# Optimization experiments

Measured on AMD Instinct MI355X. Metric: run time of the kernel, lower is better.

## Reference

```python
import jax, jax.numpy as jnp
import numpy as np

B_SZ, L, D, N = 4, 2048, 768, 16


def setup_inputs() -> dict:
    key = jax.random.key(0)
    ks = jax.random.split(key, 8)
    x = jax.random.normal(ks[0], (B_SZ, L, D), dtype=jnp.float32)
    # A_log initialized as log(arange(1..N)) repeated over d, as in the module
    A_log = jnp.log(jnp.broadcast_to(jnp.arange(1, N + 1, dtype=jnp.float32), (D, N)))
    # s_b_c: Linear(D, 2N)
    W_bc = jax.random.normal(ks[1], (2 * N, D), dtype=jnp.float32) / jnp.sqrt(D)
    b_bc = jnp.zeros((2 * N,), dtype=jnp.float32)
    # s_1: Linear(D, 1)
    W_1 = jax.random.normal(ks[2], (1, D), dtype=jnp.float32) / jnp.sqrt(D)
    b_1 = jnp.zeros((1,), dtype=jnp.float32)
    # s_delta: Linear(1, D)
    W_d = jax.random.normal(ks[3], (D, 1), dtype=jnp.float32)
    b_d = jnp.zeros((D,), dtype=jnp.float32)
    return {"x": x, "A_log": A_log, "W_bc": W_bc, "b_bc": b_bc,
            "W_1": W_1, "b_1": b_1, "W_d": W_d, "b_d": b_d}


def reference(x, A_log, W_bc, b_bc, W_1, b_1, W_d, b_d):
    b, l, d = x.shape
    n = A_log.shape[1]
    A = -jnp.exp(A_log)                                   # (d, n)
    BandC = x @ W_bc.T + b_bc                             # (b, l, 2n)
    Bm, Cm = BandC[..., :n], BandC[..., n:]               # (b, l, n) each
    # delta = softplus(s_delta(s_1(x)))  -> (b, l, d)
    s1 = x @ W_1.T + b_1                                  # (b, l, 1)
    delta = jax.nn.softplus(s1 @ W_d.T + b_d)             # (b, l, d)
    deltaA = jnp.exp(jnp.einsum('bld,dn->bldn', delta, A))        # (b, l, d, n)
    deltaB_u = jnp.einsum('bld,bln,bld->bldn', delta, Bm, x)      # (b, l, d, n)

    # sequential selective-scan over time with lax.scan
    dA_t = jnp.moveaxis(deltaA, 1, 0)      # (l, b, d, n)
    dBu_t = jnp.moveaxis(deltaB_u, 1, 0)   # (l, b, d, n)
    C_t = jnp.moveaxis(Cm, 1, 0)           # (l, b, n)

    def step(h, inp):
        dA_i, dBu_i, c_i = inp
        h = dA_i * h + dBu_i               # (b, d, n)
        y = jnp.einsum('bdn,bn->bd', h, c_i)
        return h, y

    h0 = jnp.zeros((b, d, n), dtype=x.dtype)
    _, ys = jax.lax.scan(step, h0, (dA_t, dBu_t, C_t))
    return jnp.moveaxis(ys, 0, 1)          # (b, l, d)
```

## Files before the change

kernel.cpp:

```cpp
#include <hip/hip_runtime.h>
#include <hip/hip_cooperative_groups.h>

namespace cg = cooperative_groups;

#define L_SEQ 2048
#define D_DIM 768
#define N_ST 16
#define NB 4
#define NJ 33
#define BCS 48
#define NROWS (NB * L_SEQ)
#define PROJ_ELEMS (NROWS * NJ)
#define DN (D_DIM * N_ST)

#define NCC 64
#define LCC 32
#define GS  768
#define SEGC 4
#define SCC 16

#define DSPLIT 8
#define DSEG (D_DIM / DSPLIT)
#define DK 32
#define NCHUNK (DSEG / DK)
#define RB 128
#define XST 132
#define WST 64

typedef float v2f __attribute__((ext_vector_type(2)));

__device__ __forceinline__ float fast_exp2(float x) {
#if __has_builtin(__builtin_amdgcn_exp2f)
  return __builtin_amdgcn_exp2f(x);
#else
  return __expf(x * 0.69314718055994531f);
#endif
}

__device__ __forceinline__ float softplus_f(float v) {
  float e = fast_exp2(v * 1.44269504088896f);
  float l = __log2f(1.0f + e) * 0.69314718055994531f;
  return (v > 15.0f) ? v : l;
}

__device__ __forceinline__ void pow_tree2(float e1, v2f pw2[8]) {
  float e2s = e1 * e1;
  float e4s = e2s * e2s;
  float e8s = e4s * e4s;
  v2f s2 = {e2s, e2s}, s4 = {e4s, e4s}, s8 = {e8s, e8s};
  pw2[0] = (v2f){e1, e2s};
  pw2[1] = pw2[0] * s2;
  pw2[2] = pw2[0] * s4;
  pw2[3] = pw2[1] * s4;
  pw2[4] = pw2[0] * s8;
  pw2[5] = pw2[1] * s8;
  pw2[6] = pw2[2] * s8;
  pw2[7] = pw2[3] * s8;
}

__global__ __launch_bounds__(256) void k_proj_gemm(
    const float* __restrict__ x, const float* __restrict__ W_bc,
    const float* __restrict__ W_1, float* __restrict__ PBC) {
  __shared__ float xs_t[DK * XST];
  __shared__ float ws_t[DK * WST];

  const int ds  = blockIdx.x % DSPLIT;
  const int rb0 = (blockIdx.x / DSPLIT) * RB;
  const int dbase = ds * DSEG;
  const int tid = threadIdx.x;
  const int rg = tid & 31;
  const int jg = tid >> 5;

  float acc[4][5];
#pragma unroll
  for (int i = 0; i < 4; ++i)
#pragma unroll
    for (int k = 0; k < 5; ++k) acc[i][k] = 0.0f;

  const int lrow = tid >> 1;
  const int lhalf = (tid & 1) * 16;
  const float* xg_row = x + (size_t)(rb0 + lrow) * D_DIM + dbase + lhalf;

  for (int ch = 0; ch < NCHUNK; ++ch) {
    const int dc = dbase + ch * DK;
    float4 xv[4];
#pragma unroll
    for (int q = 0; q < 4; ++q)
      xv[q] = *(const float4*)(xg_row + ch * DK + q * 4);
    float wv[8];
    int widx[8];
#pragma unroll
    for (int u = 0; u < 8; ++u) {
      int idx = tid + u * 256;
      int dk = idx >> 6, slot = idx & 63;
      int wjg = slot >> 3, wk = slot & 7;
      int j = wjg + 8 * wk;
      float v = 0.0f;
      if (wk < 5) {
        if (j < 32)       v = W_bc[(size_t)j * D_DIM + dc + dk];
        else if (j == 32) v = W_1[dc + dk];
      }
      wv[u] = v; widx[u] = dk * WST + slot;
    }
    __syncthreads();
#pragma unroll
    for (int q = 0; q < 4; ++q) {
      xs_t[(lhalf + q * 4 + 0) * XST + lrow] = xv[q].x;
      xs_t[(lhalf + q * 4 + 1) * XST + lrow] = xv[q].y;
      xs_t[(lhalf + q * 4 + 2) * XST + lrow] = xv[q].z;
      xs_t[(lhalf + q * 4 + 3) * XST + lrow] = xv[q].w;
    }
#pragma unroll
    for (int u = 0; u < 8; ++u) ws_t[widx[u]] = wv[u];
    __syncthreads();
#pragma unroll 8
    for (int dk = 0; dk < DK; ++dk) {
      float4 xr = *(const float4*)&xs_t[dk * XST + rg * 4];
      float4 wr = *(const float4*)&ws_t[dk * WST + jg * 8];
      float w4  = ws_t[dk * WST + jg * 8 + 4];
      float xa[4] = {xr.x, xr.y, xr.z, xr.w};
      float wa[5] = {wr.x, wr.y, wr.z, wr.w, w4};
#pragma unroll
      for (int i = 0; i < 4; ++i)
#pragma unroll
        for (int k = 0; k < 5; ++k)
          acc[i][k] = fmaf(xa[i], wa[k], acc[i][k]);
    }
  }

  float* pb = PBC + (size_t)ds * PROJ_ELEMS;
#pragma unroll
  for (int i = 0; i < 4; ++i) {
    int row = rb0 + rg * 4 + i;
#pragma unroll
    for (int k = 0; k < 5; ++k) {
      int j = jg + 8 * k;
      if (k < 4 || jg == 0) pb[(size_t)row * NJ + j] = acc[i][k];
    }
  }
}

__device__ __forceinline__ void phase_reduce(
    const float* __restrict__ PBC, const float* __restrict__ b_bc,
    const float* __restrict__ b_1, float* __restrict__ BC48) {
  const int t0 = blockIdx.x * 256 + threadIdx.x;
  for (int idx = t0; idx < PROJ_ELEMS; idx += GS * 256) {
    const int row = idx / NJ;
    const int j = idx - row * NJ;
    float s = 0.0f;
#pragma unroll
    for (int k = 0; k < DSPLIT; ++k) s += PBC[(size_t)k * PROJ_ELEMS + idx];
    s += (j < 32) ? b_bc[j] : b_1[0];
    BC48[(size_t)row * BCS + j] = s;
  }
}

__device__ __forceinline__ void phase_scan1(
    const float* __restrict__ x, const float* __restrict__ A_log,
    const float* __restrict__ W_d, const float* __restrict__ b_d,
    const float* __restrict__ BC48, float* __restrict__ DS,
    float* __restrict__ H) {
  const int cb = blockIdx.x % 3;
  const int c  = (blockIdx.x / 3) % NCC;
  const int b  = blockIdx.x / (3 * NCC);
  const int d  = cb * 256 + threadIdx.x;

  const float wd = W_d[d], bd = b_d[d];
  float Aln[N_ST];
  {
    const float4* al4 = (const float4*)(A_log + (size_t)d * N_ST);
#pragma unroll
    for (int q = 0; q < 4; ++q) {
      float4 v = al4[q];
      Aln[4*q+0] = -__expf(v.x) * 1.44269504088896f;
      Aln[4*q+1] = -__expf(v.y) * 1.44269504088896f;
      Aln[4*q+2] = -__expf(v.z) * 1.44269504088896f;
      Aln[4*q+3] = -__expf(v.w) * 1.44269504088896f;
    }
  }
  bool geom = true;
#pragma unroll
  for (int n = 1; n < N_ST; ++n) {
    float ref = (float)(n + 1) * Aln[0];
    geom = geom && (fabsf(Aln[n] - ref) <= 1e-4f * fabsf(ref) + 1e-12f);
  }
  const float a0 = Aln[0];

  v2f h2[8];
#pragma unroll
  for (int k = 0; k < 8; ++k) h2[k] = (v2f){0.0f, 0.0f};
  float dsum = 0.0f;

  const int l0 = c * LCC;
  const float* bc = BC48 + (size_t)(b * L_SEQ + l0) * BCS;
  const float* xp = x + (size_t)(b * L_SEQ + l0) * D_DIM + d;

  if (geom) {
#pragma unroll 8
    for (int l = 0; l < LCC; ++l) {
      const float* r = bc + l * BCS;
      float4 B0 = *(const float4*)(r + 0);
      float4 B1 = *(const float4*)(r + 4);
      float4 B2 = *(const float4*)(r + 8);
      float4 B3 = *(const float4*)(r + 12);
      float s1 = r[32];
      float delta = softplus_f(fmaf(s1, wd, bd));
      float xv = xp[(size_t)l * D_DIM];
      float f = delta * xv;
      dsum += delta;
      v2f pw2[8];
      pow_tree2(fast_exp2(a0 * delta), pw2);
      v2f f2 = {f, f};
      h2[0] = pw2[0] * h2[0] + f2 * (v2f){B0.x, B0.y};
      h2[1] = pw2[1] * h2[1] + f2 * (v2f){B0.z, B0.w};
      h2[2] = pw2[2] * h2[2] + f2 * (v2f){B1.x, B1.y};
      h2[3] = pw2[3] * h2[3] + f2 * (v2f){B1.z, B1.w};
      h2[4] = pw2[4] * h2[4] + f2 * (v2f){B2.x, B2.y};
      h2[5] = pw2[5] * h2[5] + f2 * (v2f){B2.z, B2.w};
      h2[6] = pw2[6] * h2[6] + f2 * (v2f){B3.x, B3.y};
      h2[7] = pw2[7] * h2[7] + f2 * (v2f){B3.z, B3.w};
    }
  } else {
#pragma unroll 4
    for (int l = 0; l < LCC; ++l) {
      const float* r = bc + l * BCS;
      float s1 = r[32];
      float delta = softplus_f(fmaf(s1, wd, bd));
      float f = delta * xp[(size_t)l * D_DIM];
      dsum += delta;
#pragma unroll
      for (int k = 0; k < 8; ++k) {
        h2[k].x = fmaf(fast_exp2(delta * Aln[2*k]),   h2[k].x, f * r[2*k]);
        h2[k].y = fmaf(fast_exp2(delta * Aln[2*k+1]), h2[k].y, f * r[2*k+1]);
      }
    }
  }

  DS[((size_t)b * NCC + c) * D_DIM + d] = dsum;
  size_t base = ((size_t)(b * NCC + c) * D_DIM + d) * N_ST;
  float4* H4 = (float4*)(H + base);
#pragma unroll
  for (int q = 0; q < 4; ++q)
    H4[q] = make_float4(h2[2*q].x, h2[2*q].y, h2[2*q+1].x, h2[2*q+1].y);
}

__device__ __forceinline__ void phase_combine(
    const float* __restrict__ A_log, const float* __restrict__ DS,
    float* __restrict__ H) {
  __shared__ float Pl[SEGC * 65];
  __shared__ float Hl[SEGC * 65];
  const int b    = blockIdx.x / 192;
  const int dn0  = (blockIdx.x % 192) * 64;
  const int lane = threadIdx.x & 63;
  const int j    = threadIdx.x >> 6;
  const int dn   = dn0 + lane;
  const int d    = dn >> 4;

  const float Aln1 = -__expf(A_log[dn]) * 1.44269504088896f;

  const float* dsp = DS + (size_t)b * NCC * D_DIM + d;
  float* Hp = H + (size_t)b * NCC * DN + dn;

  float p[SCC], ph[SCC];
#pragma unroll
  for (int k = 0; k < SCC; ++k) {
    const int c = j * SCC + k;
    p[k]  = fast_exp2(Aln1 * dsp[(size_t)c * D_DIM]);
    ph[k] = Hp[(size_t)c * DN];
  }

  float Pagg = 1.0f, Hagg = 0.0f;
#pragma unroll
  for (int k = 0; k < SCC; ++k) {
    Hagg = fmaf(p[k], Hagg, ph[k]);
    Pagg *= p[k];
  }

  Pl[j * 65 + lane] = Pagg;
  Hl[j * 65 + lane] = Hagg;
  __syncthreads();

  float h = 0.0f;
  for (int j2 = 0; j2 < j; ++j2)
    h = fmaf(Pl[j2 * 65 + lane], h, Hl[j2 * 65 + lane]);

#pragma unroll
  for (int k = 0; k < SCC; ++k) {
    Hp[(size_t)(j * SCC + k) * DN] = h;
    h = fmaf(p[k], h, ph[k]);
  }
}

__device__ __forceinline__ void phase_scan2(
    const float* __restrict__ x, const float* __restrict__ A_log,
    const float* __restrict__ W_d, const float* __restrict__ b_d,
    const float* __restrict__ BC48, const float* __restrict__ HIN,
    float* __restrict__ out) {
  const int cb = blockIdx.x % 3;
  const int c  = (blockIdx.x / 3) % NCC;
  const int b  = blockIdx.x / (3 * NCC);
  const int d  = cb * 256 + threadIdx.x;

  const float wd = W_d[d], bd = b_d[d];
  float Aln[N_ST];
  {
    const float4* al4 = (const float4*)(A_log + (size_t)d * N_ST);
#pragma unroll
    for (int q = 0; q < 4; ++q) {
      float4 v = al4[q];
      Aln[4*q+0] = -__expf(v.x) * 1.44269504088896f;
      Aln[4*q+1] = -__expf(v.y) * 1.44269504088896f;
      Aln[4*q+2] = -__expf(v.z) * 1.44269504088896f;
      Aln[4*q+3] = -__expf(v.w) * 1.44269504088896f;
    }
  }
  bool geom = true;
#pragma unroll
  for (int n = 1; n < N_ST; ++n) {
    float ref = (float)(n + 1) * Aln[0];
    geom = geom && (fabsf(Aln[n] - ref) <= 1e-4f * fabsf(ref) + 1e-12f);
  }
  const float a0 = Aln[0];

  v2f h2[8];
  {
    size_t base = ((size_t)(b * NCC + c) * D_DIM + d) * N_ST;
    const float4* HIN4 = (const float4*)(HIN + base);
#pragma unroll
    for (int q = 0; q < 4; ++q) {
      float4 v = HIN4[q];
      h2[2*q]   = (v2f){v.x, v.y};
      h2[2*q+1] = (v2f){v.z, v.w};
    }
  }

  const int l0 = c * LCC;
  const float* bc = BC48 + (size_t)(b * L_SEQ + l0) * BCS;
  const float* xp = x + (size_t)(b * L_SEQ + l0) * D_DIM + d;
  float* op = out + (size_t)(b * L_SEQ + l0) * D_DIM + d;

  if (geom) {
#pragma unroll 8
    for (int l = 0; l < LCC; ++l) {
      const float* r = bc + l * BCS;
      float4 B0 = *(const float4*)(r + 0);
      float4 B1 = *(const float4*)(r + 4);
      float4 B2 = *(const float4*)(r + 8);
      float4 B3 = *(const float4*)(r + 12);
      float4 C0 = *(const float4*)(r + 16);
      float4 C1 = *(const float4*)(r + 20);
      float4 C2 = *(const float4*)(r + 24);
      float4 C3 = *(const float4*)(r + 28);
      float s1 = r[32];
      float delta = softplus_f(fmaf(s1, wd, bd));
      float xv = xp[(size_t)l * D_DIM];
      float f = delta * xv;
      v2f pw2[8];
      pow_tree2(fast_exp2(a0 * delta), pw2);
      v2f f2 = {f, f};
      v2f y2 = {0.0f, 0.0f};
      h2[0] = pw2[0] * h2[0] + f2 * (v2f){B0.x, B0.y};  y2 += h2[0] * (v2f){C0.x, C0.y};
      h2[1] = pw2[1] * h2[1] + f2 * (v2f){B0.z, B0.w};  y2 += h2[1] * (v2f){C0.z, C0.w};
      h2[2] = pw2[2] * h2[2] + f2 * (v2f){B1.x, B1.y};  y2 += h2[2] * (v2f){C1.x, C1.y};
      h2[3] = pw2[3] * h2[3] + f2 * (v2f){B1.z, B1.w};  y2 += h2[3] * (v2f){C1.z, C1.w};
      h2[4] = pw2[4] * h2[4] + f2 * (v2f){B2.x, B2.y};  y2 += h2[4] * (v2f){C2.x, C2.y};
      h2[5] = pw2[5] * h2[5] + f2 * (v2f){B2.z, B2.w};  y2 += h2[5] * (v2f){C2.z, C2.w};
      h2[6] = pw2[6] * h2[6] + f2 * (v2f){B3.x, B3.y};  y2 += h2[6] * (v2f){C3.x, C3.y};
      h2[7] = pw2[7] * h2[7] + f2 * (v2f){B3.z, B3.w};  y2 += h2[7] * (v2f){C3.z, C3.w};
      op[(size_t)l * D_DIM] = y2.x + y2.y;
    }
  } else {
#pragma unroll 4
    for (int l = 0; l < LCC; ++l) {
      const float* r = bc + l * BCS;
      float s1 = r[32];
      float delta = softplus_f(fmaf(s1, wd, bd));
      float f = delta * xp[(size_t)l * D_DIM];
      float y = 0.0f;
#pragma unroll
      for (int k = 0; k < 8; ++k) {
        h2[k].x = fmaf(fast_exp2(delta * Aln[2*k]),   h2[k].x, f * r[2*k]);
        h2[k].y = fmaf(fast_exp2(delta * Aln[2*k+1]), h2[k].y, f * r[2*k+1]);
        y = fmaf(h2[k].x, r[16 + 2*k], y);
        y = fmaf(h2[k].y, r[16 + 2*k + 1], y);
      }
      op[(size_t)l * D_DIM] = y;
    }
  }
}

__global__ __launch_bounds__(256, 3) void k_mega(
    const float* __restrict__ x, const float* __restrict__ A_log,
    const float* __restrict__ W_d, const float* __restrict__ b_d,
    const float* __restrict__ PBC, const float* __restrict__ b_bc,
    const float* __restrict__ b_1, float* __restrict__ BC48,
    float* __restrict__ DS, float* __restrict__ H, float* __restrict__ out) {
  cg::grid_group grid = cg::this_grid();
  phase_reduce(PBC, b_bc, b_1, BC48);
  grid.sync();
  phase_scan1(x, A_log, W_d, b_d, BC48, DS, H);
  grid.sync();
  phase_combine(A_log, DS, H);
  grid.sync();
  phase_scan2(x, A_log, W_d, b_d, BC48, H, out);
}

__global__ __launch_bounds__(256) void k_reduce_f(
    const float* __restrict__ PBC, const float* __restrict__ b_bc,
    const float* __restrict__ b_1, float* __restrict__ BC48) {
  phase_reduce(PBC, b_bc, b_1, BC48);
}
__global__ __launch_bounds__(256, 3) void k_scan1_f(
    const float* __restrict__ x, const float* __restrict__ A_log,
    const float* __restrict__ W_d, const float* __restrict__ b_d,
    const float* __restrict__ BC48, float* __restrict__ DS,
    float* __restrict__ H) {
  phase_scan1(x, A_log, W_d, b_d, BC48, DS, H);
}
__global__ __launch_bounds__(256) void k_combine_f(
    const float* __restrict__ A_log, const float* __restrict__ DS,
    float* __restrict__ H) {
  phase_combine(A_log, DS, H);
}
__global__ __launch_bounds__(256, 3) void k_scan2_f(
    const float* __restrict__ x, const float* __restrict__ A_log,
    const float* __restrict__ W_d, const float* __restrict__ b_d,
    const float* __restrict__ BC48, const float* __restrict__ HIN,
    float* __restrict__ out) {
  phase_scan2(x, A_log, W_d, b_d, BC48, HIN, out);
}

extern "C" void kernel_launch(void* const* d_in, const int* in_sizes, int n_in,
                              void* d_out, int out_size, void* d_ws, size_t ws_size,
                              hipStream_t stream) {
  const float* x     = (const float*)d_in[0];
  const float* A_log = (const float*)d_in[1];
  const float* W_bc  = (const float*)d_in[2];
  const float* b_bc  = (const float*)d_in[3];
  const float* W_1   = (const float*)d_in[4];
  const float* b_1   = (const float*)d_in[5];
  const float* W_d   = (const float*)d_in[6];
  const float* b_d   = (const float*)d_in[7];
  float* out = (float*)d_out;
  float* ws  = (float*)d_ws;

  float* BC48 = ws;
  float* PBC  = BC48 + (size_t)NROWS * BCS;
  float* DSb  = PBC + (size_t)DSPLIT * PROJ_ELEMS;
  float* H    = DSb + (size_t)NB * NCC * D_DIM;

  k_proj_gemm<<<(NROWS / RB) * DSPLIT, 256, 0, stream>>>(x, W_bc, W_1, PBC);

  static int coop = -1;
  if (coop < 0) {
    int dev = 0;
    (void)hipGetDevice(&dev);
    int v = 0;
    (void)hipDeviceGetAttribute(&v, hipDeviceAttributeCooperativeLaunch, dev);
    coop = v ? 1 : 0;
  }

  if (coop == 1) {
    void* args[] = {(void*)&x, (void*)&A_log, (void*)&W_d, (void*)&b_d,
                    (void*)&PBC, (void*)&b_bc, (void*)&b_1,
                    (void*)&BC48, (void*)&DSb, (void*)&H, (void*)&out};
    hipError_t e = hipLaunchCooperativeKernel((const void*)k_mega, dim3(GS),
                                              dim3(256), args, 0, stream);
    if (e == hipSuccess) return;
    coop = 0;
  }

  k_reduce_f<<<GS, 256, 0, stream>>>(PBC, b_bc, b_1, BC48);
  k_scan1_f<<<GS, 256, 0, stream>>>(x, A_log, W_d, b_d, BC48, DSb, H);
  k_combine_f<<<GS, 256, 0, stream>>>(A_log, DSb, H);
  k_scan2_f<<<GS, 256, 0, stream>>>(x, A_log, W_d, b_d, BC48, H, out);
}
```

Baseline: 151.6 us.

## Reuse chunk-local outputs in scan2 and move projection reduce out of cooperative kernel

```diff
diff --git a/kernel.cpp b/kernel.cpp
--- a/kernel.cpp
+++ b/kernel.cpp
@@ -140,18 +140,63 @@
   }
 }
 
-__device__ __forceinline__ void phase_reduce(
+__global__ __launch_bounds__(256) void k_proj_reduce(
     const float* __restrict__ PBC, const float* __restrict__ b_bc,
     const float* __restrict__ b_1, float* __restrict__ BC48) {
-  const int t0 = blockIdx.x * 256 + threadIdx.x;
-  for (int idx = t0; idx < PROJ_ELEMS; idx += GS * 256) {
-    const int row = idx / NJ;
-    const int j = idx - row * NJ;
-    float s = 0.0f;
-#pragma unroll
-    for (int k = 0; k < DSPLIT; ++k) s += PBC[(size_t)k * PROJ_ELEMS + idx];
-    s += (j < 32) ? b_bc[j] : b_1[0];
-    BC48[(size_t)row * BCS + j] = s;
+  const int idx = blockIdx.x * 256 + threadIdx.x;
+  const int row = idx / NJ;
+  const int j = idx - row * NJ;
+  float s = 0.0f;
+#pragma unroll
+  for (int k = 0; k < DSPLIT; ++k) s += PBC[(size_t)k * PROJ_ELEMS + idx];
+  s += (j < 32) ? b_bc[j] : b_1[0];
+  BC48[(size_t)row * BCS + j] = s;
+}
+
+__device__ __forceinline__ void phase_combine(
+    const float* __restrict__ A_log, const float* __restrict__ DS,
+    float* __restrict__ H) {
+  __shared__ float Pl[SEGC * 65];
+  __shared__ float Hl[SEGC * 65];
+  const int b    = blockIdx.x / 192;
+  const int dn0  = (blockIdx.x % 192) * 64;
+  const int lane = threadIdx.x & 63;
+  const int j    = threadIdx.x >> 6;
+  const int dn   = dn0 + lane;
+  const int d    = dn >> 4;
+
+  const float Aln1 = -__expf(A_log[dn]) * 1.44269504088896f;
+
+  const float* dsp = DS + (size_t)b * NCC * D_DIM + d;
+  float* Hp = H + (size_t)b * NCC * DN + dn;
+
+  float p[SCC], ph[SCC];
+#pragma unroll
+  for (int k = 0; k < SCC; ++k) {
+    const int c = j * SCC + k;
+    p[k]  = fast_exp2(Aln1 * dsp[(size_t)c * D_DIM]);
+    ph[k] = Hp[(size_t)c * DN];
+  }
+
+  float Pagg = 1.0f, Hagg = 0.0f;
+#pragma unroll
+  for (int k = 0; k < SCC; ++k) {
+    Hagg = fmaf(p[k], Hagg, ph[k]);
+    Pagg *= p[k];
+  }
+
+  Pl[j * 65 + lane] = Pagg;
+  Hl[j * 65 + lane] = Hagg;
+  __syncthreads();
+
+  float h = 0.0f;
+  for (int j2 = 0; j2 < j; ++j2)
+    h = fmaf(Pl[j2 * 65 + lane], h, Hl[j2 * 65 + lane]);
+
+#pragma unroll
+  for (int k = 0; k < SCC; ++k) {
+    Hp[(size_t)(j * SCC + k) * DN] = h;
+    h = fmaf(p[k], h, ph[k]);
   }
 }
 
@@ -242,53 +287,6 @@
 #pragma unroll
   for (int q = 0; q < 4; ++q)
     H4[q] = make_float4(h2[2*q].x, h2[2*q].y, h2[2*q+1].x, h2[2*q+1].y);
-}
-
-__device__ __forceinline__ void phase_combine(
-    const float* __restrict__ A_log, const float* __restrict__ DS,
-    float* __restrict__ H) {
-  __shared__ float Pl[SEGC * 65];
-  __shared__ float Hl[SEGC * 65];
-  const int b    = blockIdx.x / 192;
-  const int dn0  = (blockIdx.x % 192) * 64;
-  const int lane = threadIdx.x & 63;
-  const int j    = threadIdx.x >> 6;
-  const int dn   = dn0 + lane;
-  const int d    = dn >> 4;
-
-  const float Aln1 = -__expf(A_log[dn]) * 1.44269504088896f;
-
-  const float* dsp = DS + (size_t)b * NCC * D_DIM + d;
-  float* Hp = H + (size_t)b * NCC * DN + dn;
-
-  float p[SCC], ph[SCC];
-#pragma unroll
-  for (int k = 0; k < SCC; ++k) {
-    const int c = j * SCC + k;
-    p[k]  = fast_exp2(Aln1 * dsp[(size_t)c * D_DIM]);
-    ph[k] = Hp[(size_t)c * DN];
-  }
-
-  float Pagg = 1.0f, Hagg = 0.0f;
-#pragma unroll
-  for (int k = 0; k < SCC; ++k) {
-    Hagg = fmaf(p[k], Hagg, ph[k]);
-    Pagg *= p[k];
-  }
-
-  Pl[j * 65 + lane] = Pagg;
-  Hl[j * 65 + lane] = Hagg;
-  __syncthreads();
-
-  float h = 0.0f;
-  for (int j2 = 0; j2 < j; ++j2)
-    h = fmaf(Pl[j2 * 65 + lane], h, Hl[j2 * 65 + lane]);
-
-#pragma unroll
-  for (int k = 0; k < SCC; ++k) {
-    Hp[(size_t)(j * SCC + k) * DN] = h;
-    h = fmaf(p[k], h, ph[k]);
-  }
 }
 
 __device__ __forceinline__ void phase_scan2(
@@ -389,27 +387,166 @@
   }
 }
 
-__global__ __launch_bounds__(256, 3) void k_mega(
+__global__ __launch_bounds__(256, 3) void k_scan_mega(
     const float* __restrict__ x, const float* __restrict__ A_log,
     const float* __restrict__ W_d, const float* __restrict__ b_d,
-    const float* __restrict__ PBC, const float* __restrict__ b_bc,
-    const float* __restrict__ b_1, float* __restrict__ BC48,
-    float* __restrict__ DS, float* __restrict__ H, float* __restrict__ out) {
+    const float* __restrict__ BC48, float* __restrict__ DS,
+    float* __restrict__ H, float* __restrict__ out) {
   cg::grid_group grid = cg::this_grid();
-  phase_reduce(PBC, b_bc, b_1, BC48);
-  grid.sync();
-  phase_scan1(x, A_log, W_d, b_d, BC48, DS, H);
+
+  const int cb = blockIdx.x % 3;
+  const int c  = (blockIdx.x / 3) % NCC;
+  const int b  = blockIdx.x / (3 * NCC);
+  const int d  = cb * 256 + threadIdx.x;
+
+  const float wd = W_d[d], bd = b_d[d];
+  float Aln[N_ST];
+  {
+    const float4* al4 = (const float4*)(A_log + (size_t)d * N_ST);
+#pragma unroll
+    for (int q = 0; q < 4; ++q) {
+      float4 v = al4[q];
+      Aln[4*q+0] = -__expf(v.x) * 1.44269504088896f;
+      Aln[4*q+1] = -__expf(v.y) * 1.44269504088896f;
+      Aln[4*q+2] = -__expf(v.z) * 1.44269504088896f;
+      Aln[4*q+3] = -__expf(v.w) * 1.44269504088896f;
+    }
+  }
+  bool geom = true;
+#pragma unroll
+  for (int n = 1; n < N_ST; ++n) {
+    float ref = (float)(n + 1) * Aln[0];
+    geom = geom && (fabsf(Aln[n] - ref) <= 1e-4f * fabsf(ref) + 1e-12f);
+  }
+  const float a0 = Aln[0];
+
+  const int l0 = c * LCC;
+  const float* bc = BC48 + (size_t)(b * L_SEQ + l0) * BCS;
+  const float* xp = x + (size_t)(b * L_SEQ + l0) * D_DIM + d;
+  float* op = out + (size_t)(b * L_SEQ + l0) * D_DIM + d;
+
+  float yl[LCC];
+  v2f h2[8];
+#pragma unroll
+  for (int k = 0; k < 8; ++k) h2[k] = (v2f){0.0f, 0.0f};
+  float dsum = 0.0f;
+
+  if (geom) {
+#pragma unroll
+    for (int l = 0; l < LCC; ++l) {
+      const float* r = bc + l * BCS;
+      float4 B0 = *(const float4*)(r + 0);
+      float4 B1 = *(const float4*)(r + 4);
+      float4 B2 = *(const float4*)(r + 8);
+      float4 B3 = *(const float4*)(r + 12);
+      float4 C0 = *(const float4*)(r + 16);
+      float4 C1 = *(const float4*)(r + 20);
+      float4 C2 = *(const float4*)(r + 24);
+      float4 C3 = *(const float4*)(r + 28);
+      float s1 = r[32];
+      float delta = softplus_f(fmaf(s1, wd, bd));
+      float xv = xp[(size_t)l * D_DIM];
+      float f = delta * xv;
+      dsum += delta;
+      v2f pw2[8];
+      pow_tree2(fast_exp2(a0 * delta), pw2);
+      v2f f2 = {f, f};
+      v2f y2 = {0.0f, 0.0f};
+      h2[0] = pw2[0] * h2[0] + f2 * (v2f){B0.x, B0.y};  y2 += h2[0] * (v2f){C0.x, C0.y};
+      h2[1] = pw2[1] * h2[1] + f2 * (v2f){B0.z, B0.w};  y2 += h2[1] * (v2f){C0.z, C0.w};
+      h2[2] = pw2[2] * h2[2] + f2 * (v2f){B1.x, B1.y};  y2 += h2[2] * (v2f){C1.x, C1.y};
+      h2[3] = pw2[3] * h2[3] + f2 * (v2f){B1.z, B1.w};  y2 += h2[3] * (v2f){C1.z, C1.w};
+      h2[4] = pw2[4] * h2[4] + f2 * (v2f){B2.x, B2.y};  y2 += h2[4] * (v2f){C2.x, C2.y};
+      h2[5] = pw2[5] * h2[5] + f2 * (v2f){B2.z, B2.w};  y2 += h2[5] * (v2f){C2.z, C2.w};
+      h2[6] = pw2[6] * h2[6] + f2 * (v2f){B3.x, B3.y};  y2 += h2[6] * (v2f){C3.x, C3.y};
+      h2[7] = pw2[7] * h2[7] + f2 * (v2f){B3.z, B3.w};  y2 += h2[7] * (v2f){C3.z, C3.w};
+      yl[l] = y2.x + y2.y;
+    }
+  } else {
+#pragma unroll 4
+    for (int l = 0; l < LCC; ++l) {
+      const float* r = bc + l * BCS;
+      float s1 = r[32];
+      float delta = softplus_f(fmaf(s1, wd, bd));
+      float f = delta * xp[(size_t)l * D_DIM];
+      dsum += delta;
+#pragma unroll
+      for (int k = 0; k < 8; ++k) {
+        h2[k].x = fmaf(fast_exp2(delta * Aln[2*k]),   h2[k].x, f * r[2*k]);
+        h2[k].y = fmaf(fast_exp2(delta * Aln[2*k+1]), h2[k].y, f * r[2*k+1]);
+      }
+    }
+  }
+
+  DS[((size_t)b * NCC + c) * D_DIM + d] = dsum;
+  {
+    size_t base = ((size_t)(b * NCC + c) * D_DIM + d) * N_ST;
+    float4* H4 = (float4*)(H + base);
+#pragma unroll
+    for (int q = 0; q < 4; ++q)
+      H4[q] = make_float4(h2[2*q].x, h2[2*q].y, h2[2*q+1].x, h2[2*q+1].y);
+  }
+
   grid.sync();
   phase_combine(A_log, DS, H);
   grid.sync();
-  phase_scan2(x, A_log, W_d, b_d, BC48, H, out);
-}
-
-__global__ __launch_bounds__(256) void k_reduce_f(
-    const float* __restrict__ PBC, const float* __restrict__ b_bc,
-    const float* __restrict__ b_1, float* __restrict__ BC48) {
-  phase_reduce(PBC, b_bc, b_1, BC48);
-}
+
+  v2f hin2[8];
+  {
+    size_t base = ((size_t)(b * NCC + c) * D_DIM + d) * N_ST;
+    const float4* HIN4 = (const float4*)(H + base);
+#pragma unroll
+    for (int q = 0; q < 4; ++q) {
+      float4 v = HIN4[q];
+      hin2[2*q]   = (v2f){v.x, v.y};
+      hin2[2*q+1] = (v2f){v.z, v.w};
+    }
+  }
+
+  if (geom) {
+    float logE = 0.0f;
+#pragma unroll
+    for (int l = 0; l < LCC; ++l) {
+      const float* r = bc + l * BCS;
+      float delta = softplus_f(fmaf(r[32], wd, bd));
+      logE = fmaf(a0, delta, logE);
+      v2f pw2[8];
+      pow_tree2(fast_exp2(logE), pw2);
+      float4 C0 = *(const float4*)(r + 16);
+      float4 C1 = *(const float4*)(r + 20);
+      float4 C2 = *(const float4*)(r + 24);
+      float4 C3 = *(const float4*)(r + 28);
+      v2f y2 = {0.0f, 0.0f};
+      y2 += (hin2[0] * pw2[0]) * (v2f){C0.x, C0.y};
+      y2 += (hin2[1] * pw2[1]) * (v2f){C0.z, C0.w};
+      y2 += (hin2[2] * pw2[2]) * (v2f){C1.x, C1.y};
+      y2 += (hin2[3] * pw2[3]) * (v2f){C1.z, C1.w};
+      y2 += (hin2[4] * pw2[4]) * (v2f){C2.x, C2.y};
+      y2 += (hin2[5] * pw2[5]) * (v2f){C2.z, C2.w};
+      y2 += (hin2[6] * pw2[6]) * (v2f){C3.x, C3.y};
+      y2 += (hin2[7] * pw2[7]) * (v2f){C3.z, C3.w};
+      op[(size_t)l * D_DIM] = yl[l] + y2.x + y2.y;
+    }
+  } else {
+#pragma unroll 4
+    for (int l = 0; l < LCC; ++l) {
+      const float* r = bc + l * BCS;
+      float s1 = r[32];
+      float delta = softplus_f(fmaf(s1, wd, bd));
+      float f = delta * xp[(size_t)l * D_DIM];
+      float y = 0.0f;
+#pragma unroll
+      for (int k = 0; k < 8; ++k) {
+        hin2[k].x = fmaf(fast_exp2(delta * Aln[2*k]),   hin2[k].x, f * r[2*k]);
+        hin2[k].y = fmaf(fast_exp2(delta * Aln[2*k+1]), hin2[k].y, f * r[2*k+1]);
+        y = fmaf(hin2[k].x, r[16 + 2*k], y);
+        y = fmaf(hin2[k].y, r[16 + 2*k + 1], y);
+      }
+      op[(size_t)l * D_DIM] = y;
+    }
+  }
+}
+
 __global__ __launch_bounds__(256, 3) void k_scan1_f(
     const float* __restrict__ x, const float* __restrict__ A_log,
     const float* __restrict__ W_d, const float* __restrict__ b_d,
@@ -450,6 +587,7 @@
   float* H    = DSb + (size_t)NB * NCC * D_DIM;
 
   k_proj_gemm<<<(NROWS / RB) * DSPLIT, 256, 0, stream>>>(x, W_bc, W_1, PBC);
+  k_proj_reduce<<<(PROJ_ELEMS + 255) / 256, 256, 0, stream>>>(PBC, b_bc, b_1, BC48);
 
   static int coop = -1;
   if (coop < 0) {
@@ -462,15 +600,13 @@
 
   if (coop == 1) {
     void* args[] = {(void*)&x, (void*)&A_log, (void*)&W_d, (void*)&b_d,
-                    (void*)&PBC, (void*)&b_bc, (void*)&b_1,
                     (void*)&BC48, (void*)&DSb, (void*)&H, (void*)&out};
-    hipError_t e = hipLaunchCooperativeKernel((const void*)k_mega, dim3(GS),
+    hipError_t e = hipLaunchCooperativeKernel((const void*)k_scan_mega, dim3(GS),
                                               dim3(256), args, 0, stream);
     if (e == hipSuccess) return;
     coop = 0;
   }
 
-  k_reduce_f<<<GS, 256, 0, stream>>>(PBC, b_bc, b_1, BC48);
   k_scan1_f<<<GS, 256, 0, stream>>>(x, A_log, W_d, b_d, BC48, DSb, H);
   k_combine_f<<<GS, 256, 0, stream>>>(A_log, DSb, H);
   k_scan2_f<<<GS, 256, 0, stream>>>(x, A_log, W_d, b_d, BC48, H, out);
```

After: 150.4 us. No clear change (-0.8%).
